# Optimization experiments

Measured on AMD Instinct MI355X. Metric: run time of the kernel, lower is better.

## Reference

```python
import jax, jax.numpy as jnp
import numpy as np


def setup_inputs() -> dict:
    key = jax.random.key(0)
    ks = jax.random.split(key, 10)
    B, E, D, T, K = 256, 1024, 256, 256, 128
    s_gru = 1.0 / np.sqrt(E)
    s_tok = 1.0 / np.sqrt(D)
    return {
        "c": jax.random.normal(ks[0], (B, E), jnp.float32),
        "K": K,
        "x": jax.random.normal(ks[1], (B, D, T), jnp.float32),
        # GRU params (torch layout: rows ordered [reset, update, new])
        "W_ih": jax.random.uniform(ks[2], (3 * E, E), jnp.float32, -s_gru, s_gru),
        "W_hh": jax.random.uniform(ks[3], (3 * E, E), jnp.float32, -s_gru, s_gru),
        "b_ih": jax.random.uniform(ks[4], (3 * E,), jnp.float32, -s_gru, s_gru),
        "b_hh": jax.random.uniform(ks[5], (3 * E,), jnp.float32, -s_gru, s_gru),
        # input tokenizer: Linear(D -> E)
        "W_tok": jax.random.uniform(ks[6], (E, D), jnp.float32, -s_tok, s_tok),
        "b_tok": jax.random.uniform(ks[7], (E,), jnp.float32, -s_tok, s_tok),
        # untokenizer: Linear(E -> D)
        "W_untok": jax.random.uniform(ks[8], (D, E), jnp.float32, -s_gru, s_gru),
        "b_untok": jax.random.uniform(ks[9], (D,), jnp.float32, -s_gru, s_gru),
    }


def reference(c, K, x, W_ih, W_hh, b_ih, b_hh, W_tok, b_tok, W_untok, b_untok):
    B, E = c.shape
    # Teacher-forced inputs: step 0 uses zeros, step k>0 uses tokenized x[:, :, T-K+k-1].
    x_tf = jnp.swapaxes(x[:, :, -K:], 1, 2)            # [B, K, D]
    tok = x_tf @ W_tok.T + b_tok                        # [B, K, E]
    inputs = jnp.concatenate(
        [jnp.zeros((B, 1, E), c.dtype), tok[:, : K - 1]], axis=1
    )                                                   # [B, K, E]
    # Precompute all input-side gate projections (parallel across steps).
    gi = inputs @ W_ih.T + b_ih                         # [B, K, 3E]
    gi = jnp.swapaxes(gi, 0, 1)                         # [K, B, 3E]

    def step(h, gi_k):
        gi_r, gi_z, gi_n = jnp.split(gi_k, 3, axis=-1)
        gh = h @ W_hh.T + b_hh                          # [B, 3E]
        gh_r, gh_z, gh_n = jnp.split(gh, 3, axis=-1)
        r = jax.nn.sigmoid(gi_r + gh_r)
        z = jax.nn.sigmoid(gi_z + gh_z)
        n = jnp.tanh(gi_n + r * gh_n)
        h_new = (1.0 - z) * n + z * h
        return h_new, h_new

    _, ys = jax.lax.scan(step, c, gi)                   # ys: [K, B, E]
    y = jnp.swapaxes(ys, 0, 1)                          # [B, K, E]
    y = y @ W_untok.T + b_untok                         # [B, K, D]
    return jnp.swapaxes(y, 1, 2)                        # [B, D, K]
```

## Files before the change

### kernel.cpp

```cpp
#include <hip/hip_runtime.h>
#include <cstdint>

typedef __attribute__((ext_vector_type(8))) short bf16x8;
typedef __attribute__((ext_vector_type(4))) float f32x4;
typedef unsigned short u16;
typedef unsigned long long u64;

__device__ __forceinline__ u16 f2bf(float x) {
  unsigned u = __builtin_bit_cast(unsigned, x);
  return (u16)((u + 0x7FFFu + ((u >> 16) & 1u)) >> 16);
}
__device__ __forceinline__ float bf2f(u16 h) {
  unsigned u = ((unsigned)h) << 16;
  return __builtin_bit_cast(float, u);
}
__device__ __forceinline__ f32x4 mfma16(bf16x8 a, bf16x8 b, f32x4 c) {
  return __builtin_amdgcn_mfma_f32_16x16x32_bf16(a, b, c, 0, 0, 0);
}

__device__ __forceinline__ bf16x8 ld_coh8(const u16* p) {
  u64 a = __hip_atomic_load((const u64*)p, __ATOMIC_RELAXED, __HIP_MEMORY_SCOPE_AGENT);
  u64 b = __hip_atomic_load((const u64*)(p + 4), __ATOMIC_RELAXED, __HIP_MEMORY_SCOPE_AGENT);
  ulonglong2 t;
  t.x = a;
  t.y = b;
  return __builtin_bit_cast(bf16x8, t);
}
__device__ __forceinline__ void st_coh16(u16* p, uint4 v) {
  ulonglong2 t = __builtin_bit_cast(ulonglong2, v);
  __hip_atomic_store((u64*)p, t.x, __ATOMIC_RELAXED, __HIP_MEMORY_SCOPE_AGENT);
  __hip_atomic_store((u64*)(p + 4), t.y, __ATOMIC_RELAXED, __HIP_MEMORY_SCOPE_AGENT);
}

__device__ __forceinline__ size_t pidx(int r, int k, int KC) {
  return ((size_t)((r >> 4) * KC + (k >> 5))) * 512 +
         (size_t)(((((k & 31) >> 3) << 4) | (r & 15)) * 8) + (size_t)(k & 7);
}
__device__ __forceinline__ int rowperm(int p, int e) {
  return (((e >> 4) * 3 + p) << 4) + (e & 15);
}

__global__ void k_round(const float* __restrict__ whh, const float* __restrict__ wun,
                        u16* __restrict__ whhp, u16* __restrict__ wunp) {
  int i = blockIdx.x * 256 + threadIdx.x, st = 1024 * 256;
  for (int j = i; j < 3072 * 1024; j += st) {
    int r = j >> 10, k = j & 1023;
    int p = r >> 10, e = r & 1023;
    whhp[pidx(rowperm(p, e), k, 32)] = f2bf(whh[j]);
  }
  for (int j = i; j < 256 * 1024; j += st) {
    int r = j >> 10, k = j & 1023;
    wunp[pidx(r, k, 32)] = f2bf(wun[j]);
  }
}

__global__ void k_hinit(const float* __restrict__ c, u16* __restrict__ hhi,
                        u16* __restrict__ hlo) {
  int i = blockIdx.x * 256 + threadIdx.x;
  int b = i >> 10, e = i & 1023;
  float v = c[i];
  u16 hi = f2bf(v);
  size_t o = pidx(b, e, 32);
  hhi[o] = hi;
  hlo[o] = f2bf(v - bf2f(hi));
}

__global__ void k_zero(unsigned* __restrict__ bar) {
  bar[blockIdx.x * 256 + threadIdx.x] = 0u;
}

__global__ void k_wcomb(const float* __restrict__ wih, const float* __restrict__ wtok,
                        u16* __restrict__ wcb) {
  __shared__ float la[64][33];
  __shared__ float lb[32][65];
  int i0 = blockIdx.x << 6, j0 = blockIdx.y << 6;
  int tid = threadIdx.x;
  int ty = tid >> 4, tx = tid & 15;
  float acc[4][4] = {};
  for (int k0 = 0; k0 < 1024; k0 += 32) {
    __syncthreads();
#pragma unroll
    for (int i = 0; i < 8; ++i) {
      int r = (tid >> 5) + i * 8, cc = tid & 31;
      la[r][cc] = wih[(size_t)(i0 + r) * 1024 + k0 + cc];
    }
#pragma unroll
    for (int i = 0; i < 8; ++i) {
      int idx = i * 256 + tid;
      int r = idx >> 6, cc = idx & 63;
      lb[r][cc] = wtok[(size_t)(k0 + r) * 256 + j0 + cc];
    }
    __syncthreads();
#pragma unroll
    for (int kk = 0; kk < 32; ++kk) {
      float av[4], bv[4];
#pragma unroll
      for (int ii = 0; ii < 4; ++ii) av[ii] = la[ty * 4 + ii][kk];
#pragma unroll
      for (int jj = 0; jj < 4; ++jj) bv[jj] = lb[kk][tx * 4 + jj];
#pragma unroll
      for (int ii = 0; ii < 4; ++ii)
#pragma unroll
        for (int jj = 0; jj < 4; ++jj) acc[ii][jj] += av[ii] * bv[jj];
    }
  }
#pragma unroll
  for (int ii = 0; ii < 4; ++ii)
#pragma unroll
    for (int jj = 0; jj < 4; ++jj) {
      int r = i0 + ty * 4 + ii;
      int p = r >> 10, e = r & 1023;
      wcb[pidx(rowperm(p, e), j0 + tx * 4 + jj, 8)] = f2bf(acc[ii][jj]);
    }
}

__global__ void k_bcomb(const float* __restrict__ wih, const float* __restrict__ btok,
                        const float* __restrict__ bih, float* __restrict__ bc) {
  __shared__ float red[256];
  int j = blockIdx.x, t = threadIdx.x;
  float s = 0.f;
  for (int e = t; e < 1024; e += 256) s += wih[(size_t)j * 1024 + e] * btok[e];
  red[t] = s;
  __syncthreads();
  for (int off = 128; off > 0; off >>= 1) {
    if (t < off) red[t] += red[t + off];
    __syncthreads();
  }
  if (t == 0) bc[j] = red[0] + bih[j];
}

__global__ void k_xprep(const float* __restrict__ x, u16* __restrict__ xhi,
                        u16* __restrict__ xlo) {
  __shared__ float t[64][129];
  int bid = blockIdx.x;
  int b = bid >> 2, d0 = (bid & 3) << 6;
  int tid = threadIdx.x;
#pragma unroll
  for (int i = 0; i < 32; ++i) {
    int idx = i * 256 + tid;
    int dd = idx >> 7, tt = idx & 127;
    t[dd][tt] = x[(size_t)b * 65536 + (size_t)(d0 + dd) * 256 + 128 + tt];
  }
  __syncthreads();
#pragma unroll
  for (int i = 0; i < 32; ++i) {
    int idx = i * 256 + tid;
    int dd = idx & 63, kk = idx >> 6;
    if (kk < 127) {
      float v = t[dd][kk];
      u16 hi = f2bf(v);
      size_t o = (size_t)(kk + 1) * 65536 + pidx(b, d0 + dd, 8);
      xhi[o] = hi;
      xlo[o] = f2bf(v - bf2f(hi));
    }
  }
}

__launch_bounds__(512, 1)
__global__ void k_gru5(u16* __restrict__ hhi, u16* __restrict__ hlo,
                       const u16* __restrict__ xhi, const u16* __restrict__ xlo,
                       const u16* __restrict__ whp, const u16* __restrict__ wcp,
                       const float* __restrict__ bih, const float* __restrict__ bcb,
                       const float* __restrict__ bhh, u16* __restrict__ ys,
                       unsigned* __restrict__ bar) {
  __shared__ __align__(16) u16 lwh[3][32][512];
  __shared__ __align__(16) u16 lwc[3][8][512];
  __shared__ __align__(16) float red[2][8][256];
  __shared__ __align__(16) u16 sth[32][40];
  __shared__ __align__(16) u16 stl[32][40];
  __shared__ u16 hold_h[32][36];
  __shared__ u16 hold_l[32][36];

  int bid = blockIdx.x;
  int g = bid & 7, q = bid >> 3;
  int tid = threadIdx.x;
  int w = tid >> 6, lane = tid & 63, l15 = lane & 15, l4 = lane >> 4;
  int mw = w & 1, ks = w >> 1;

  {
    const u16* s1 = whp + (size_t)(6 * q) * 32 * 512;
    u16* d1 = &lwh[0][0][0];
#pragma unroll
    for (int i = 0; i < 12; ++i)
      *(uint4*)(d1 + i * 4096 + tid * 8) = *(const uint4*)(s1 + i * 4096 + tid * 8);
    const u16* s2 = wcp + (size_t)(6 * q) * 8 * 512;
    u16* d2 = &lwc[0][0][0];
#pragma unroll
    for (int i = 0; i < 3; ++i)
      *(uint4*)(d2 + i * 4096 + tid * 8) = *(const uint4*)(s2 + i * 4096 + tid * 8);
  }
  __syncthreads();

  float bAr[2], bAz[2], bAn[2], bBr[2], bBz[2], bBn[2], bhn_[2];
#pragma unroll
  for (int eb = 0; eb < 2; ++eb) {
    int e = q * 32 + eb * 16 + l15;
    float hr = bhh[e], hz = bhh[1024 + e];
    bhn_[eb] = bhh[2048 + e];
    bAr[eb] = bih[e] + hr;
    bAz[eb] = bih[1024 + e] + hz;
    bAn[eb] = bih[2048 + e];
    bBr[eb] = bcb[e] + hr;
    bBz[eb] = bcb[1024 + e] + hz;
    bBn[eb] = bcb[2048 + e];
  }

  unsigned* myflag = bar + (size_t)(g * 32 + q) * 16;
  const unsigned* pollflag = bar + (size_t)(g * 32 + (lane & 31)) * 16;

  int rg = g * 2 + mw;
  const u16* Bs0 = whp + (size_t)(6 * q + 3) * 32 * 512 + (size_t)(lane * 8);
  const u16* Bs1 = whp + (size_t)(6 * q + 4) * 32 * 512 + (size_t)(lane * 8);
  const u16* Bs2 = whp + (size_t)(6 * q + 5) * 32 * 512 + (size_t)(lane * 8);
  const u16* Cs0 = wcp + (size_t)(6 * q + 3) * 8 * 512 + (size_t)(lane * 8);
  const u16* Cs1 = wcp + (size_t)(6 * q + 4) * 8 * 512 + (size_t)(lane * 8);
  const u16* Cs2 = wcp + (size_t)(6 * q + 5) * 8 * 512 + (size_t)(lane * 8);

  for (int k = 0; k < 128; ++k) {
    int cur = k & 1, nxt = cur ^ 1;

    f32x4 R0{}, Z0{}, N0{}, X0{}, R1{}, Z1{}, N1{}, X1{};

    bf16x8 pb0[8], pb1[8], pb2[8];
#pragma unroll
    for (int c = 0; c < 8; ++c) {
      int kk = ks * 8 + c;
      pb0[c] = *(const bf16x8*)(Bs0 + (size_t)kk * 512);
      pb1[c] = *(const bf16x8*)(Bs1 + (size_t)kk * 512);
      pb2[c] = *(const bf16x8*)(Bs2 + (size_t)kk * 512);
    }

    if (k > 0) {
      const u16* Xh = xhi + (size_t)k * 65536 + (size_t)rg * 4096 + (size_t)(lane * 8);
      const u16* Xl = xlo + (size_t)k * 65536 + (size_t)rg * 4096 + (size_t)(lane * 8);
#pragma unroll
      for (int c = 0; c < 2; ++c) {
        int kc = ks * 2 + c;
        bf16x8 ah = *(const bf16x8*)(Xh + (size_t)kc * 512);
        bf16x8 al = *(const bf16x8*)(Xl + (size_t)kc * 512);
        bf16x8 c00 = *(const bf16x8*)&lwc[0][kc][lane * 8];
        bf16x8 c10 = *(const bf16x8*)&lwc[1][kc][lane * 8];
        bf16x8 c20 = *(const bf16x8*)&lwc[2][kc][lane * 8];
        bf16x8 c01 = *(const bf16x8*)(Cs0 + (size_t)kc * 512);
        bf16x8 c11 = *(const bf16x8*)(Cs1 + (size_t)kc * 512);
        bf16x8 c21 = *(const bf16x8*)(Cs2 + (size_t)kc * 512);
        R0 = mfma16(ah, c00, R0); R0 = mfma16(al, c00, R0);
        Z0 = mfma16(ah, c10, Z0); Z0 = mfma16(al, c10, Z0);
        X0 = mfma16(ah, c20, X0); X0 = mfma16(al, c20, X0);
        R1 = mfma16(ah, c01, R1); R1 = mfma16(al, c01, R1);
        Z1 = mfma16(ah, c11, Z1); Z1 = mfma16(al, c11, Z1);
        X1 = mfma16(ah, c21, X1); X1 = mfma16(al, c21, X1);
      }
      if (w == 0) {
        while (true) {
          unsigned v = __hip_atomic_load(pollflag, __ATOMIC_RELAXED,
                                         __HIP_MEMORY_SCOPE_AGENT);
          if (__all((int)(v >= (unsigned)k))) break;
          __builtin_amdgcn_s_sleep(2);
        }
      }
      __syncthreads();
    }

    const u16* Hh = hhi + (size_t)cur * 262144 + (size_t)rg * 16384 + (size_t)(lane * 8);
    bf16x8 ahv[8];
#pragma unroll
    for (int c = 0; c < 8; ++c)
      ahv[c] = ld_coh8(Hh + (size_t)(ks * 8 + c) * 512);

#pragma unroll
    for (int c = 0; c < 8; ++c) {
      int kk = ks * 8 + c;
      bf16x8 b00 = *(const bf16x8*)&lwh[0][kk][lane * 8];
      bf16x8 b10 = *(const bf16x8*)&lwh[1][kk][lane * 8];
      bf16x8 b20 = *(const bf16x8*)&lwh[2][kk][lane * 8];
      R0 = mfma16(ahv[c], b00, R0);
      Z0 = mfma16(ahv[c], b10, Z0);
      N0 = mfma16(ahv[c], b20, N0);
      R1 = mfma16(ahv[c], pb0[c], R1);
      Z1 = mfma16(ahv[c], pb1[c], Z1);
      N1 = mfma16(ahv[c], pb2[c], N1);
    }

    if (ks == 3) {
      size_t ho = (size_t)cur * 262144 + (size_t)(rg * 32 + q) * 512 + (size_t)(lane * 8);
      bf16x8 hh = ld_coh8(hhi + ho);
      bf16x8 hl = ld_coh8(hlo + ho);
      int r15 = lane & 15, oct = lane >> 4;
#pragma unroll
      for (int j = 0; j < 8; ++j) {
        hold_h[mw * 16 + r15][oct * 8 + j] = (u16)hh[j];
        hold_l[mw * 16 + r15][oct * 8 + j] = (u16)hl[j];
      }
      *(f32x4*)&red[mw][0][lane * 4] = R0;
      *(f32x4*)&red[mw][1][lane * 4] = Z0;
      *(f32x4*)&red[mw][2][lane * 4] = N0;
      *(f32x4*)&red[mw][3][lane * 4] = X0;
      *(f32x4*)&red[mw][4][lane * 4] = R1;
      *(f32x4*)&red[mw][5][lane * 4] = Z1;
      *(f32x4*)&red[mw][6][lane * 4] = N1;
      *(f32x4*)&red[mw][7][lane * 4] = X1;
    }
    __syncthreads();
    if (ks == 2) {
      *(f32x4*)&red[mw][0][lane * 4] = R0 + *(const f32x4*)&red[mw][0][lane * 4];
      *(f32x4*)&red[mw][1][lane * 4] = Z0 + *(const f32x4*)&red[mw][1][lane * 4];
      *(f32x4*)&red[mw][2][lane * 4] = N0 + *(const f32x4*)&red[mw][2][lane * 4];
      *(f32x4*)&red[mw][3][lane * 4] = X0 + *(const f32x4*)&red[mw][3][lane * 4];
      *(f32x4*)&red[mw][4][lane * 4] = R1 + *(const f32x4*)&red[mw][4][lane * 4];
      *(f32x4*)&red[mw][5][lane * 4] = Z1 + *(const f32x4*)&red[mw][5][lane * 4];
      *(f32x4*)&red[mw][6][lane * 4] = N1 + *(const f32x4*)&red[mw][6][lane * 4];
      *(f32x4*)&red[mw][7][lane * 4] = X1 + *(const f32x4*)&red[mw][7][lane * 4];
    }
    __syncthreads();
    if (ks == 1) {
      *(f32x4*)&red[mw][0][lane * 4] = R0 + *(const f32x4*)&red[mw][0][lane * 4];
      *(f32x4*)&red[mw][1][lane * 4] = Z0 + *(const f32x4*)&red[mw][1][lane * 4];
      *(f32x4*)&red[mw][2][lane * 4] = N0 + *(const f32x4*)&red[mw][2][lane * 4];
      *(f32x4*)&red[mw][3][lane * 4] = X0 + *(const f32x4*)&red[mw][3][lane * 4];
      *(f32x4*)&red[mw][4][lane * 4] = R1 + *(const f32x4*)&red[mw][4][lane * 4];
      *(f32x4*)&red[mw][5][lane * 4] = Z1 + *(const f32x4*)&red[mw][5][lane * 4];
      *(f32x4*)&red[mw][6][lane * 4] = N1 + *(const f32x4*)&red[mw][6][lane * 4];
      *(f32x4*)&red[mw][7][lane * 4] = X1 + *(const f32x4*)&red[mw][7][lane * 4];
    }
    __syncthreads();
    if (ks == 0) {
      f32x4 vR0 = R0 + *(const f32x4*)&red[mw][0][lane * 4];
      f32x4 vZ0 = Z0 + *(const f32x4*)&red[mw][1][lane * 4];
      f32x4 vN0 = N0 + *(const f32x4*)&red[mw][2][lane * 4];
      f32x4 vX0 = X0 + *(const f32x4*)&red[mw][3][lane * 4];
      f32x4 vR1 = R1 + *(const f32x4*)&red[mw][4][lane * 4];
      f32x4 vZ1 = Z1 + *(const f32x4*)&red[mw][5][lane * 4];
      f32x4 vN1 = N1 + *(const f32x4*)&red[mw][6][lane * 4];
      f32x4 vX1 = X1 + *(const f32x4*)&red[mw][7][lane * 4];
#pragma unroll
      for (int eb = 0; eb < 2; ++eb) {
        f32x4 vR = eb ? vR1 : vR0;
        f32x4 vZ = eb ? vZ1 : vZ0;
        f32x4 vN = eb ? vN1 : vN0;
        f32x4 vX = eb ? vX1 : vX0;
        float bir = k ? bBr[eb] : bAr[eb];
        float biz = k ? bBz[eb] : bAz[eb];
        float bin = k ? bBn[eb] : bAn[eb];
        int e64 = eb * 16 + l15;
#pragma unroll
        for (int j = 0; j < 4; ++j) {
          int row_rel = mw * 16 + l4 * 4 + j;
          float hold = bf2f(hold_h[row_rel][e64]) + bf2f(hold_l[row_rel][e64]);
          float gr = vR[j] + bir;
          float gz = vZ[j] + biz;
          float gh = vN[j] + bhn_[eb];
          float gx = vX[j] + bin;
          float r = 1.f / (1.f + __expf(-gr));
          float z = 1.f / (1.f + __expf(-gz));
          float n = 1.f - 2.f / (1.f + __expf(2.f * (gx + r * gh)));
          float h = (1.f - z) * n + z * hold;
          u16 hi = f2bf(h);
          sth[row_rel][e64] = hi;
          stl[row_rel][e64] = f2bf(h - bf2f(hi));
        }
      }
    }
    __syncthreads();

    if (tid < 256) {
      int mws = (tid >> 6) & 1, isLo = tid >> 7, l = tid & 63;
      int r15 = l & 15, oct = l >> 4;
      size_t off = (size_t)((g * 2 + mws) * 32 + q) * 512 + (size_t)(l * 8);
      const u16* src = isLo ? &stl[mws * 16 + r15][oct * 8] : &sth[mws * 16 + r15][oct * 8];
      u16* dst = (isLo ? hlo : hhi) + (size_t)nxt * 262144;
      st_coh16(dst + off, *(const uint4*)src);
    } else if (tid < 384) {
      int cc = tid - 256;
      int b_rel = cc >> 2, oct = cc & 3;
      size_t f = (size_t)((g * 32 + b_rel) * 8 + (k >> 4)) * 32 + (size_t)q;
      *(uint4*)(ys + f * 512 + (size_t)(((oct << 4) | (k & 15)) * 8)) =
          *(const uint4*)&sth[b_rel][oct * 8];
    }

    if (k < 127) {
      __syncthreads();
      if (tid == 0)
        __hip_atomic_store(myflag, (unsigned)(k + 1), __ATOMIC_RELAXED,
                           __HIP_MEMORY_SCOPE_AGENT);
    }
  }
}

__launch_bounds__(256, 4)
__global__ void k_untok3(const u16* __restrict__ ysp, const u16* __restrict__ wunp,
                         const float* __restrict__ bun, float* __restrict__ out) {
  int bid = blockIdx.x;
  int mtile = bid >> 1, dh = bid & 1;
  int b = mtile >> 1, kk0 = (mtile & 1) << 6;
  int w = threadIdx.x >> 6, lane = threadIdx.x & 63, l15 = lane & 15, l4 = lane >> 4;
  int rg = mtile * 4 + w;
  const u16* A = ysp + (size_t)rg * 16384 + (size_t)(lane * 8);
  f32x4 acc[8] = {};
  float bv[8];
#pragma unroll
  for (int nt = 0; nt < 8; ++nt) bv[nt] = bun[dh * 128 + nt * 16 + l15];
#pragma unroll 4
  for (int kc = 0; kc < 32; ++kc) {
    bf16x8 a = *(const bf16x8*)(A + (size_t)kc * 512);
#pragma unroll
    for (int nt = 0; nt < 8; ++nt) {
      const u16* B = wunp + ((size_t)((dh * 8 + nt) * 32 + kc)) * 512 + (size_t)(lane * 8);
      acc[nt] = mfma16(a, *(const bf16x8*)B, acc[nt]);
    }
  }
#pragma unroll
  for (int nt = 0; nt < 8; ++nt) {
    float4 v = {acc[nt][0] + bv[nt], acc[nt][1] + bv[nt], acc[nt][2] + bv[nt],
                acc[nt][3] + bv[nt]};
    int d = dh * 128 + nt * 16 + l15;
    *(float4*)(out + (size_t)b * 32768 + (size_t)d * 128 + kk0 + w * 16 + l4 * 4) = v;
  }
}

extern "C" void kernel_launch(void* const* d_in, const int* in_sizes, int n_in,
                              void* d_out, int out_size, void* d_ws, size_t ws_size,
                              hipStream_t stream) {
  const float* c_in = (const float*)d_in[0];
  const float* x_in = (const float*)d_in[2];
  const float* Wih  = (const float*)d_in[3];
  const float* Whh  = (const float*)d_in[4];
  const float* bih  = (const float*)d_in[5];
  const float* bhh  = (const float*)d_in[6];
  const float* Wtok = (const float*)d_in[7];
  const float* btok = (const float*)d_in[8];
  const float* Wun  = (const float*)d_in[9];
  const float* bun  = (const float*)d_in[10];
  float* out = (float*)d_out;
  char* ws = (char*)d_ws;

  const size_t OW_HH = 0;
  const size_t OW_C  = 6291456;
  const size_t OW_UN = 7864320;
  const size_t OBC   = 8388608;
  const size_t OXHI  = 8400896;
  const size_t OXLO  = 25178112;
  const size_t OHHI  = 41955328;
  const size_t OHLO  = 43003904;
  const size_t OYS   = 44052480;
  const size_t OBAR  = 111161344;
  const size_t NEED  = 111177728;
  if (ws_size < NEED) return;

  u16* whh_p = (u16*)(ws + OW_HH);
  u16* wc_p  = (u16*)(ws + OW_C);
  u16* wun_p = (u16*)(ws + OW_UN);
  float* bc  = (float*)(ws + OBC);
  u16* xhi   = (u16*)(ws + OXHI);
  u16* xlo   = (u16*)(ws + OXLO);
  u16* hhi   = (u16*)(ws + OHHI);
  u16* hlo   = (u16*)(ws + OHLO);
  u16* ys    = (u16*)(ws + OYS);
  unsigned* bar = (unsigned*)(ws + OBAR);

  k_round<<<1024, 256, 0, stream>>>(Whh, Wun, whh_p, wun_p);
  k_wcomb<<<dim3(48, 4), 256, 0, stream>>>(Wih, Wtok, wc_p);
  k_bcomb<<<3072, 256, 0, stream>>>(Wih, btok, bih, bc);
  k_xprep<<<1024, 256, 0, stream>>>(x_in, xhi, xlo);
  k_hinit<<<1024, 256, 0, stream>>>(c_in, hhi, hlo);
  k_zero<<<16, 256, 0, stream>>>(bar);

  {
    u16* hhi_l = hhi;
    u16* hlo_l = hlo;
    const u16* xhi_l = xhi;
    const u16* xlo_l = xlo;
    const u16* whp_l = whh_p;
    const u16* wcp_l = wc_p;
    const float* bih_l = bih;
    const float* bc_l = bc;
    const float* bhh_l = bhh;
    u16* ys_l = ys;
    unsigned* bar_l = bar;
    void* args[] = {&hhi_l, &hlo_l, &xhi_l, &xlo_l, &whp_l, &wcp_l,
                    &bih_l, &bc_l, &bhh_l, &ys_l, &bar_l};
    hipLaunchCooperativeKernel((const void*)k_gru5, dim3(256), dim3(512), args, 0, stream);
  }

  k_untok3<<<1024, 256, 0, stream>>>(ys, wun_p, bun, out);
}
```

Before: 905.9 us.

## Map GRU blocks to XCC groups and use sc0 vector loads for hidden state

Each block reads its hardware XCC id and takes a slot from an atomic counter, so the batch group g matches the XCD and hidden-state exchange stays within one XCD's L2. The paired 64-bit atomic loads and stores of h are replaced with single dwordx4 loads carrying the sc0 cache bit and plain 128-bit stores. All h loads, including the old-h loads, are issued together ahead of one waitcnt. The risks are coherence: plain stores and sc0 loads must still make h visible across blocks, which only holds if every XCC gets exactly 32 blocks so that slots never collide.

Result: faster. 820.3 us (-9.4%).

```diff
diff --git a/kernel.cpp b/kernel.cpp
--- a/kernel.cpp
+++ b/kernel.cpp
@@ -17,19 +17,10 @@
 __device__ __forceinline__ f32x4 mfma16(bf16x8 a, bf16x8 b, f32x4 c) {
   return __builtin_amdgcn_mfma_f32_16x16x32_bf16(a, b, c, 0, 0, 0);
 }
-
-__device__ __forceinline__ bf16x8 ld_coh8(const u16* p) {
-  u64 a = __hip_atomic_load((const u64*)p, __ATOMIC_RELAXED, __HIP_MEMORY_SCOPE_AGENT);
-  u64 b = __hip_atomic_load((const u64*)(p + 4), __ATOMIC_RELAXED, __HIP_MEMORY_SCOPE_AGENT);
-  ulonglong2 t;
-  t.x = a;
-  t.y = b;
-  return __builtin_bit_cast(bf16x8, t);
-}
-__device__ __forceinline__ void st_coh16(u16* p, uint4 v) {
-  ulonglong2 t = __builtin_bit_cast(ulonglong2, v);
-  __hip_atomic_store((u64*)p, t.x, __ATOMIC_RELAXED, __HIP_MEMORY_SCOPE_AGENT);
-  __hip_atomic_store((u64*)(p + 4), t.y, __ATOMIC_RELAXED, __HIP_MEMORY_SCOPE_AGENT);
+__device__ __forceinline__ bf16x8 bc8(uint4 v) { return __builtin_bit_cast(bf16x8, v); }
+
+__device__ __forceinline__ void ld_sc0(const u16* p, uint4& v) {
+  asm volatile("global_load_dwordx4 %0, %1, off sc0" : "=v"(v) : "v"(p));
 }
 
 __device__ __forceinline__ size_t pidx(int r, int k, int KC) {
@@ -170,10 +161,21 @@
   __shared__ __align__(16) u16 stl[32][40];
   __shared__ u16 hold_h[32][36];
   __shared__ u16 hold_l[32][36];
-
-  int bid = blockIdx.x;
-  int g = bid & 7, q = bid >> 3;
+  __shared__ int s_gq[2];
+
   int tid = threadIdx.x;
+  if (tid == 0) {
+    unsigned xcc;
+    asm volatile("s_getreg_b32 %0, hwreg(HW_REG_XCC_ID)" : "=s"(xcc));
+    xcc &= 7u;
+    unsigned slot = __hip_atomic_fetch_add(bar + 4096 + xcc, 1u, __ATOMIC_RELAXED,
+                                           __HIP_MEMORY_SCOPE_AGENT);
+    s_gq[0] = (int)xcc;
+    s_gq[1] = (int)(slot & 31u);
+  }
+  __syncthreads();
+  int g = s_gq[0], q = s_gq[1];
+
   int w = tid >> 6, lane = tid & 63, l15 = lane & 15, l4 = lane >> 4;
   int mw = w & 1, ks = w >> 1;
 
@@ -263,29 +265,37 @@
     }
 
     const u16* Hh = hhi + (size_t)cur * 262144 + (size_t)rg * 16384 + (size_t)(lane * 8);
-    bf16x8 ahv[8];
+    uint4 ahr[8];
+    uint4 hhr{}, hlr{};
+    __builtin_amdgcn_sched_barrier(0);
 #pragma unroll
     for (int c = 0; c < 8; ++c)
-      ahv[c] = ld_coh8(Hh + (size_t)(ks * 8 + c) * 512);
+      ld_sc0(Hh + (size_t)(ks * 8 + c) * 512, ahr[c]);
+    if (ks == 3) {
+      size_t ho = (size_t)cur * 262144 + (size_t)(rg * 32 + q) * 512 + (size_t)(lane * 8);
+      ld_sc0(hhi + ho, hhr);
+      ld_sc0(hlo + ho, hlr);
+    }
+    asm volatile("s_waitcnt vmcnt(0)" ::: "memory");
+    __builtin_amdgcn_sched_barrier(0);
 
 #pragma unroll
     for (int c = 0; c < 8; ++c) {
       int kk = ks * 8 + c;
+      bf16x8 a = bc8(ahr[c]);
       bf16x8 b00 = *(const bf16x8*)&lwh[0][kk][lane * 8];
       bf16x8 b10 = *(const bf16x8*)&lwh[1][kk][lane * 8];
       bf16x8 b20 = *(const bf16x8*)&lwh[2][kk][lane * 8];
-      R0 = mfma16(ahv[c], b00, R0);
-      Z0 = mfma16(ahv[c], b10, Z0);
-      N0 = mfma16(ahv[c], b20, N0);
-      R1 = mfma16(ahv[c], pb0[c], R1);
-      Z1 = mfma16(ahv[c], pb1[c], Z1);
-      N1 = mfma16(ahv[c], pb2[c], N1);
+      R0 = mfma16(a, b00, R0);
+      Z0 = mfma16(a, b10, Z0);
+      N0 = mfma16(a, b20, N0);
+      R1 = mfma16(a, pb0[c], R1);
+      Z1 = mfma16(a, pb1[c], Z1);
+      N1 = mfma16(a, pb2[c], N1);
     }
 
     if (ks == 3) {
-      size_t ho = (size_t)cur * 262144 + (size_t)(rg * 32 + q) * 512 + (size_t)(lane * 8);
-      bf16x8 hh = ld_coh8(hhi + ho);
-      bf16x8 hl = ld_coh8(hlo + ho);
+      bf16x8 hh = bc8(hhr), hl = bc8(hlr);
       int r15 = lane & 15, oct = lane >> 4;
 #pragma unroll
       for (int j = 0; j < 8; ++j) {
@@ -369,7 +379,7 @@
       size_t off = (size_t)((g * 2 + mws) * 32 + q) * 512 + (size_t)(l * 8);
       const u16* src = isLo ? &stl[mws * 16 + r15][oct * 8] : &sth[mws * 16 + r15][oct * 8];
       u16* dst = (isLo ? hlo : hhi) + (size_t)nxt * 262144;
-      st_coh16(dst + off, *(const uint4*)src);
+      *(uint4*)(dst + off) = *(const uint4*)src;
     } else if (tid < 384) {
       int cc = tid - 256;
       int b_rel = cc >> 2, oct = cc & 3;
@@ -444,7 +454,7 @@
   const size_t OHLO  = 43003904;
   const size_t OYS   = 44052480;
   const size_t OBAR  = 111161344;
-  const size_t NEED  = 111177728;
+  const size_t NEED  = 111178752;
   if (ws_size < NEED) return;
 
   u16* whh_p = (u16*)(ws + OW_HH);
@@ -463,7 +473,7 @@
   k_bcomb<<<3072, 256, 0, stream>>>(Wih, btok, bih, bc);
   k_xprep<<<1024, 256, 0, stream>>>(x_in, xhi, xlo);
   k_hinit<<<1024, 256, 0, stream>>>(c_in, hhi, hlo);
-  k_zero<<<16, 256, 0, stream>>>(bar);
+  k_zero<<<17, 256, 0, stream>>>(bar);
 
   {
     u16* hhi_l = hhi;
```
